# Performance work log

Measured on AMD Instinct MI355X. Metric: run time of the kernel, lower is better.

Reference implementation:

```python
import jax, jax.numpy as jnp
import numpy as np

R = 0.4          # ball radius
K = 32           # max_neighbors
S = 512          # cluster_num
BN_EPS = 1e-5


def fps(data, npoint):
    """Furthest point sampling. data: [B,N,C] -> idx [B,npoint] int32.
    Deterministic start at index 0 (original uses randint)."""
    B, N, C = data.shape

    def step(carry, _):
        dist, far = carry
        cent = jnp.take_along_axis(data, far[:, None, None], axis=1)  # [B,1,C]
        d = jnp.sum((data - cent) ** 2, -1)                           # [B,N]
        dist = jnp.minimum(dist, d)
        new_far = jnp.argmax(dist, -1).astype(jnp.int32)
        return (dist, new_far), far

    dist0 = jnp.full((B, N), 1e10, data.dtype)
    far0 = jnp.zeros((B,), jnp.int32)
    _, idxs = jax.lax.scan(step, (dist0, far0), None, length=npoint)
    return idxs.T  # [B,npoint]


def gather_points(data, idx):
    """data [B,N,C], idx [B,S] -> [B,S,C]"""
    return jnp.take_along_axis(data, idx[..., None], axis=1)


def gather_groups(data, idx):
    """data [B,N,C], idx [B,S,K] -> [B,S,K,C]"""
    B, N, C = data.shape
    _, Sq, Kq = idx.shape
    flat = jnp.take_along_axis(data, idx.reshape(B, Sq * Kq)[..., None], axis=1)
    return flat.reshape(B, Sq, Kq, C)


def square_dist(a, b):
    """a [B,N,C], b [B,M,C] -> [B,N,M]"""
    return (-2.0 * jnp.einsum('bnc,bmc->bnm', a, b)
            + jnp.sum(a ** 2, -1)[:, :, None]
            + jnp.sum(b ** 2, -1)[:, None, :])


def knn_query(data, query, max_neighbors, r):
    """Ball query: indices of up to max_neighbors points within r, padded with
    the first valid index. data [B,N,C], query [B,S,C] -> [B,S,K] int32."""
    B, N, _ = data.shape
    d = square_dist(query, data)                              # [B,S,N]
    idx = jnp.where(d <= r * r, jnp.arange(N, dtype=jnp.int32)[None, None, :], N)
    idx = jnp.sort(idx, axis=-1)[:, :, :max_neighbors]        # ascending, N = invalid
    first = idx[:, :, :1]
    return jnp.where(idx == N, first, idx)


def mlp_layer(x, w, b, g, be):
    """1x1 Conv2d + BatchNorm2d (training-mode batch stats) + ReLU.
    x [B,S,K,Cin], w [Cout,Cin] -> [B,S,K,Cout]"""
    y = jnp.einsum('bskc,oc->bsko', x, w) + b
    m = jnp.mean(y, axis=(0, 1, 2))
    v = jnp.var(y, axis=(0, 1, 2))
    y = (y - m) * jax.lax.rsqrt(v + BN_EPS) * g + be
    return jax.nn.relu(y)


def setup_inputs() -> dict:
    key = jax.random.key(0)
    ks = jax.random.split(key, 5)
    B, N = 16, 8192
    data = jax.random.normal(ks[0], (B, N, 3), jnp.float32)
    data_feature = jax.random.normal(ks[1], (B, N, 3), jnp.float32)
    w0 = jax.random.normal(ks[2], (64, 6), jnp.float32) * 0.1
    w1 = jax.random.normal(ks[3], (64, 64), jnp.float32) * 0.1
    w2 = jax.random.normal(ks[4], (128, 64), jnp.float32) * 0.1
    zeros = lambda c: jnp.zeros((c,), jnp.float32)
    ones = lambda c: jnp.ones((c,), jnp.float32)
    return dict(data=data, data_feature=data_feature,
                w0=w0, b0=zeros(64), g0=ones(64), be0=zeros(64),
                w1=w1, b1=zeros(64), g1=ones(64), be1=zeros(64),
                w2=w2, b2=zeros(128), g2=ones(128), be2=zeros(128))


def reference(data, data_feature, w0, b0, g0, be0, w1, b1, g1, be1, w2, b2, g2, be2):
    B, N, C = data.shape
    fps_idx = fps(data, S)                              # [B,S]
    centroids = gather_points(data, fps_idx)            # [B,S,3]
    nbr_idx = knn_query(data, centroids, K, R)          # [B,S,K]
    sample = gather_groups(data, nbr_idx)               # [B,S,K,3]
    sample_norm = sample - centroids[:, :, None, :]
    feat = gather_groups(data_feature, nbr_idx)         # [B,S,K,3]
    x = jnp.concatenate([sample_norm, feat], axis=-1)   # [B,S,K,6]
    x = mlp_layer(x, w0, b0, g0, be0)
    x = mlp_layer(x, w1, b1, g1, be1)
    x = mlp_layer(x, w2, b2, g2, be2)
    out = jnp.max(x, axis=2)                            # [B,S,128]
    return centroids, out
```

## Files before the change

### kernel.cpp

```cpp
#include <hip/hip_runtime.h>
#include <math.h>

constexpr int Bc = 16;
constexpr int Nc = 8192;
constexpr int Sc = 512;
constexpr int Kc = 32;
constexpr int Pc = Bc * Sc * Kc;

__global__ __launch_bounds__(256, 1)
void fps_kernel(const float* __restrict__ data,
                float* __restrict__ cent_out,
                float* __restrict__ cent_ws) {
  const int b = blockIdx.x;
  const int t = threadIdx.x;
  const int lane = t & 63, w = t >> 6;

  __shared__ float lx[Nc], ly[Nc], lz[Nc];
  __shared__ unsigned long long red_k[2][4];
  __shared__ int idx_hist[Sc];

  const float* db = data + (size_t)b * Nc * 3;

  float px[32], py[32], pz[32], dist[32];
#pragma unroll
  for (int j = 0; j < 32; ++j) {
    int p = t + 256 * j;
    px[j] = db[p * 3 + 0];
    py[j] = db[p * 3 + 1];
    pz[j] = db[p * 3 + 2];
    dist[j] = 1e10f;
    lx[p] = px[j]; ly[p] = py[j]; lz[p] = pz[j];
  }
  __syncthreads();

  int far = 0;
  for (int it = 0; it < Sc; ++it) {
    const int sfar = __builtin_amdgcn_readfirstlane(far);
    if (t == 0) idx_hist[it] = sfar;
    const float cx = lx[sfar];
    const float cy = ly[sfar];
    const float cz = lz[sfar];

    float best = -1.0f; int bj = 0;
#pragma unroll
    for (int j = 0; j < 32; ++j) {
      float dx = __fsub_rn(px[j], cx);
      float dy = __fsub_rn(py[j], cy);
      float dz = __fsub_rn(pz[j], cz);
      float d = __fadd_rn(__fadd_rn(__fmul_rn(dx, dx), __fmul_rn(dy, dy)),
                          __fmul_rn(dz, dz));
      float nd = fminf(dist[j], d);
      dist[j] = nd;
      if (nd > best) { best = nd; bj = j; }
    }
    const int bidx = t + 256 * bj;

    float wmax = best;
#pragma unroll
    for (int off = 32; off; off >>= 1) wmax = fmaxf(wmax, __shfl_xor(wmax, off));

    unsigned long long m = __ballot(best == wmax);
    int idx;
    if (__popcll(m) == 1) {
      idx = __shfl(bidx, (int)__ffsll((long long)m) - 1);
    } else {
      int cand = (best == wmax) ? bidx : 0x7fffffff;
#pragma unroll
      for (int off = 32; off; off >>= 1) cand = min(cand, __shfl_xor(cand, off));
      idx = cand;
    }

    unsigned long long key =
        ((unsigned long long)__float_as_uint(wmax) << 32) |
        (unsigned long long)(0xFFFFFFFFu - (unsigned)idx);
    const int par = it & 1;
    if (lane == 0) red_k[par][w] = key;
    __syncthreads();

    unsigned long long kk = red_k[par][lane & 3];
    {
      unsigned long long o1 = __shfl_xor(kk, 1);
      kk = (o1 > kk) ? o1 : kk;
      unsigned long long o2 = __shfl_xor(kk, 2);
      kk = (o2 > kk) ? o2 : kk;
    }
    far = (int)(0xFFFFFFFFu - (unsigned)(kk & 0xFFFFFFFFull));
  }

  __syncthreads();
  for (int s = t; s < Sc; s += 256) {
    int id = idx_hist[s];
    float cx = lx[id], cy = ly[id], cz = lz[id];
    size_t o = ((size_t)b * Sc + s) * 3;
    cent_out[o + 0] = cx; cent_out[o + 1] = cy; cent_out[o + 2] = cz;
    cent_ws[o + 0]  = cx; cent_ws[o + 1]  = cy; cent_ws[o + 2]  = cz;
  }
}

__global__ __launch_bounds__(256)
void ball_kernel(const float* __restrict__ data,
                 const float* __restrict__ feat,
                 const float* __restrict__ cent_ws,
                 float* __restrict__ x0) {
  const int w = threadIdx.x >> 6, lane = threadIdx.x & 63;
  const int q = blockIdx.x * 4 + w;
  const int b = q >> 9;
  const float* db = data + (size_t)b * Nc * 3;
  const float* fb = feat + (size_t)b * Nc * 3;

  const float qx = cent_ws[q * 3 + 0];
  const float qy = cent_ws[q * 3 + 1];
  const float qz = cent_ws[q * 3 + 2];
  const float q2 = __fadd_rn(__fadd_rn(__fmul_rn(qx, qx), __fmul_rn(qy, qy)),
                             __fmul_rn(qz, qz));

  __shared__ int nbr[4][Kc];
  int have = 0;
  for (int base = 0; base < Nc; base += 64) {
    int i = base + lane;
    float px = db[i * 3 + 0], py = db[i * 3 + 1], pz = db[i * 3 + 2];
    float p2 = __fadd_rn(__fadd_rn(__fmul_rn(px, px), __fmul_rn(py, py)),
                         __fmul_rn(pz, pz));
    float dt = fmaf(qz, pz, fmaf(qy, py, __fmul_rn(qx, px)));
    float d = __fadd_rn(__fadd_rn(__fmul_rn(-2.0f, dt), q2), p2);
    bool ok = d <= 0.16f;
    unsigned long long mask = __ballot(ok);
    if (mask) {
      int pos = have + __popcll(mask & ((1ull << lane) - 1ull));
      if (ok && pos < Kc) nbr[w][pos] = i;
      have += __popcll(mask);
      if (have >= Kc) break;
    }
  }
  if (have > Kc) have = Kc;
  __syncthreads();

  if (lane < Kc) {
    int k = lane;
    int j = nbr[w][k < have ? k : 0];
    float sx = __fsub_rn(db[j * 3 + 0], qx);
    float sy = __fsub_rn(db[j * 3 + 1], qy);
    float sz = __fsub_rn(db[j * 3 + 2], qz);
    float fx = fb[j * 3 + 0], fy = fb[j * 3 + 1], fz = fb[j * 3 + 2];
    size_t pidx = (size_t)q * Kc + k;
    x0[(size_t)0 * Pc + pidx] = sx;
    x0[(size_t)1 * Pc + pidx] = sy;
    x0[(size_t)2 * Pc + pidx] = sz;
    x0[(size_t)3 * Pc + pidx] = fx;
    x0[(size_t)4 * Pc + pidx] = fy;
    x0[(size_t)5 * Pc + pidx] = fz;
  }
}

__global__ __launch_bounds__(256)
void pass_a(const float* __restrict__ x0, const float* __restrict__ w0,
            const float* __restrict__ b0, float* __restrict__ part0) {
  const int lane = threadIdx.x & 63, w = threadIdx.x >> 6;
  const int slice = blockIdx.x * 4 + w;
  const int o = lane;
  float W[6];
#pragma unroll
  for (int c = 0; c < 6; ++c) W[c] = w0[o * 6 + c];
  const float bias = b0[o];
  float sum = 0.f, sq = 0.f;
  const int pps = Pc / 4096;
  const int p0 = slice * pps;
  for (int j = 0; j < pps; ++j) {
    int p = p0 + j;
    float y = bias;
#pragma unroll
    for (int c = 0; c < 6; ++c) y = fmaf(x0[(size_t)c * Pc + p], W[c], y);
    sum += y;
    sq = fmaf(y, y, sq);
  }
  __shared__ float bsum[64], bsq[64];
  if (threadIdx.x < 64) { bsum[threadIdx.x] = 0.f; bsq[threadIdx.x] = 0.f; }
  __syncthreads();
  atomicAdd(&bsum[o], sum);
  atomicAdd(&bsq[o], sq);
  __syncthreads();
  if (threadIdx.x < 64)       part0[blockIdx.x * 128 + threadIdx.x] = bsum[threadIdx.x];
  else if (threadIdx.x < 128) part0[blockIdx.x * 128 + threadIdx.x] = bsq[threadIdx.x - 64];
}

__global__ __launch_bounds__(256)
void reduce_k(const float* __restrict__ part, int nblk, int nch,
              const float* __restrict__ g, const float* __restrict__ be,
              float* __restrict__ AB) {
  const int o = blockIdx.x;
  const int t = threadIdx.x;
  double sum = 0.0, sq = 0.0;
  for (int i = t; i < nblk; i += 256) {
    sum += (double)part[(size_t)i * (2 * nch) + o];
    sq  += (double)part[(size_t)i * (2 * nch) + nch + o];
  }
  __shared__ double ls[256], lq[256];
  ls[t] = sum; lq[t] = sq;
  __syncthreads();
  for (int s = 128; s > 0; s >>= 1) {
    if (t < s) { ls[t] += ls[t + s]; lq[t] += lq[t + s]; }
    __syncthreads();
  }
  if (t == 0) {
    double m = ls[0] / (double)Pc;
    double v = lq[0] / (double)Pc - m * m;
    double A = (double)g[o] / sqrt(v + 1e-5);
    AB[o] = (float)A;
    AB[nch + o] = (float)((double)be[o] - m * A);
  }
}

__global__ __launch_bounds__(256)
void pass_b(const float* __restrict__ x0, const float* __restrict__ w0,
            const float* __restrict__ b0, const float* __restrict__ AB0,
            const float* __restrict__ w1, const float* __restrict__ b1,
            float* __restrict__ y1, float* __restrict__ part1) {
  const int p = blockIdx.x * 256 + threadIdx.x;
  const int lane = threadIdx.x & 63, w = threadIdx.x >> 6;

  float xin[6];
#pragma unroll
  for (int c = 0; c < 6; ++c) xin[c] = x0[(size_t)c * Pc + p];

  float x1[64];
#pragma unroll
  for (int o = 0; o < 64; ++o) {
    float y = b0[o];
#pragma unroll
    for (int c = 0; c < 6; ++c) y = fmaf(xin[c], w0[o * 6 + c], y);
    x1[o] = fmaxf(fmaf(y, AB0[o], AB0[64 + o]), 0.f);
  }

  __shared__ float ssum[4][64][17], ssq[4][64][17];

  for (int o = 0; o < 64; ++o) {
    float a0 = b1[o], a1 = 0.f, a2 = 0.f, a3 = 0.f;
#pragma unroll
    for (int c = 0; c < 64; c += 4) {
      a0 = fmaf(x1[c + 0], w1[o * 64 + c + 0], a0);
      a1 = fmaf(x1[c + 1], w1[o * 64 + c + 1], a1);
      a2 = fmaf(x1[c + 2], w1[o * 64 + c + 2], a2);
      a3 = fmaf(x1[c + 3], w1[o * 64 + c + 3], a3);
    }
    float acc = (a0 + a1) + (a2 + a3);
    y1[(size_t)o * Pc + p] = acc;

    float sv = acc + __shfl_xor(acc, 1);
    sv += __shfl_xor(sv, 2);
    float q = acc * acc;
    float qv = q + __shfl_xor(q, 1);
    qv += __shfl_xor(qv, 2);
    if ((lane & 3) == 0) {
      ssum[w][o][lane >> 2] = sv;
      ssq[w][o][lane >> 2] = qv;
    }
  }
  __syncthreads();
  if (threadIdx.x < 128) {
    const int o = threadIdx.x & 63;
    const bool isq = threadIdx.x >= 64;
    float s = 0.f;
#pragma unroll
    for (int ww = 0; ww < 4; ++ww)
      for (int k = 0; k < 16; ++k)
        s += isq ? ssq[ww][o][k] : ssum[ww][o][k];
    part1[blockIdx.x * 128 + threadIdx.x] = s;
  }
}

__global__ __launch_bounds__(256)
void pass_c(const float* __restrict__ y1, const float* __restrict__ AB1,
            const float* __restrict__ w2, const float* __restrict__ b2,
            float* __restrict__ maxy2, float* __restrict__ part2) {
  const int p = blockIdx.x * 256 + threadIdx.x;
  const int lane = threadIdx.x & 63, w = threadIdx.x >> 6;
  const int grp = p >> 5;

  float x2[64];
#pragma unroll
  for (int c = 0; c < 64; ++c) {
    float v = y1[(size_t)c * Pc + p];
    x2[c] = fmaxf(fmaf(v, AB1[c], AB1[64 + c]), 0.f);
  }

  __shared__ float ssum[4][128][9], ssq[4][128][9];

  for (int o = 0; o < 128; ++o) {
    float a0 = b2[o], a1 = 0.f, a2 = 0.f, a3 = 0.f;
#pragma unroll
    for (int c = 0; c < 64; c += 4) {
      a0 = fmaf(x2[c + 0], w2[o * 64 + c + 0], a0);
      a1 = fmaf(x2[c + 1], w2[o * 64 + c + 1], a1);
      a2 = fmaf(x2[c + 2], w2[o * 64 + c + 2], a2);
      a3 = fmaf(x2[c + 3], w2[o * 64 + c + 3], a3);
    }
    float acc = (a0 + a1) + (a2 + a3);

    float mx = acc;
#pragma unroll
    for (int off = 16; off > 0; off >>= 1) mx = fmaxf(mx, __shfl_xor(mx, off));
    if ((lane & 31) == 0) maxy2[(size_t)grp * 128 + o] = mx;

    float sv = acc + __shfl_xor(acc, 1);
    sv += __shfl_xor(sv, 2);
    sv += __shfl_xor(sv, 4);
    float q = acc * acc;
    float qv = q + __shfl_xor(q, 1);
    qv += __shfl_xor(qv, 2);
    qv += __shfl_xor(qv, 4);
    if ((lane & 7) == 0) {
      ssum[w][o][lane >> 3] = sv;
      ssq[w][o][lane >> 3] = qv;
    }
  }
  __syncthreads();
  {
    const int o = threadIdx.x & 127;
    const bool isq = threadIdx.x >= 128;
    float s = 0.f;
#pragma unroll
    for (int ww = 0; ww < 4; ++ww)
      for (int k = 0; k < 8; ++k)
        s += isq ? ssq[ww][o][k] : ssum[ww][o][k];
    part2[blockIdx.x * 256 + threadIdx.x] = s;
  }
}

__global__ __launch_bounds__(256)
void final_k(const float* __restrict__ maxy2, const float* __restrict__ AB2,
             float* __restrict__ out) {
  int i = blockIdx.x * 256 + threadIdx.x;
  int o = i & 127;
  out[i] = fmaxf(fmaf(maxy2[i], AB2[o], AB2[128 + o]), 0.f);
}

extern "C" void kernel_launch(void* const* d_in, const int* in_sizes, int n_in,
                              void* d_out, int out_size, void* d_ws, size_t ws_size,
                              hipStream_t stream) {
  const float* data = (const float*)d_in[0];
  const float* feat = (const float*)d_in[1];
  const float* w0 = (const float*)d_in[2];
  const float* b0 = (const float*)d_in[3];
  const float* g0 = (const float*)d_in[4];
  const float* be0 = (const float*)d_in[5];
  const float* w1 = (const float*)d_in[6];
  const float* b1 = (const float*)d_in[7];
  const float* g1 = (const float*)d_in[8];
  const float* be1 = (const float*)d_in[9];
  const float* w2 = (const float*)d_in[10];
  const float* b2 = (const float*)d_in[11];
  const float* g2 = (const float*)d_in[12];
  const float* be2 = (const float*)d_in[13];
  float* out = (float*)d_out;

  float* ws = (float*)d_ws;
  float* cent_ws = ws; ws += (size_t)Bc * Sc * 3;
  float* x0 = ws;      ws += (size_t)6 * Pc;
  float* y1 = ws;      ws += (size_t)64 * Pc;
  float* maxy2 = ws;   ws += (size_t)Bc * Sc * 128;
  float* part0 = ws;   ws += 1024 * 128;
  float* part1 = ws;   ws += 1024 * 128;
  float* part2 = ws;   ws += 1024 * 256;
  float* AB0 = ws;     ws += 128;
  float* AB1 = ws;     ws += 128;
  float* AB2 = ws;     ws += 256;

  fps_kernel<<<Bc, 256, 0, stream>>>(data, out, cent_ws);
  ball_kernel<<<(Bc * Sc) / 4, 256, 0, stream>>>(data, feat, cent_ws, x0);
  pass_a<<<1024, 256, 0, stream>>>(x0, w0, b0, part0);
  reduce_k<<<64, 256, 0, stream>>>(part0, 1024, 64, g0, be0, AB0);
  pass_b<<<Pc / 256, 256, 0, stream>>>(x0, w0, b0, AB0, w1, b1, y1, part1);
  reduce_k<<<64, 256, 0, stream>>>(part1, 1024, 64, g1, be1, AB1);
  pass_c<<<Pc / 256, 256, 0, stream>>>(y1, AB1, w2, b2, maxy2, part2);
  reduce_k<<<128, 256, 0, stream>>>(part2, 1024, 128, g2, be2, AB2);
  final_k<<<(Bc * Sc * 128) / 256, 256, 0, stream>>>(maxy2, AB2, out + (size_t)Bc * Sc * 3);
}
```

Measured before the change: 869.3 us.

## Recompute layer-1 activations in pass_c instead of storing y1; DPP reductions in FPS

```diff
diff --git a/kernel.cpp b/kernel.cpp
--- a/kernel.cpp
+++ b/kernel.cpp
@@ -6,6 +6,12 @@
 constexpr int Sc = 512;
 constexpr int Kc = 32;
 constexpr int Pc = Bc * Sc * Kc;
+
+template <int CTRL>
+__device__ __forceinline__ float dpp_max_stage(float x) {
+  int p = __builtin_amdgcn_update_dpp(0, __float_as_int(x), CTRL, 0xf, 0xf, true);
+  return fmaxf(x, __int_as_float(p));
+}
 
 __global__ __launch_bounds__(256, 1)
 void fps_kernel(const float* __restrict__ data,
@@ -56,8 +62,12 @@
     const int bidx = t + 256 * bj;
 
     float wmax = best;
-#pragma unroll
-    for (int off = 32; off; off >>= 1) wmax = fmaxf(wmax, __shfl_xor(wmax, off));
+    wmax = dpp_max_stage<0xB1>(wmax);
+    wmax = dpp_max_stage<0x4E>(wmax);
+    wmax = dpp_max_stage<0x141>(wmax);
+    wmax = dpp_max_stage<0x140>(wmax);
+    wmax = fmaxf(wmax, __shfl_xor(wmax, 16));
+    wmax = fmaxf(wmax, __shfl_xor(wmax, 32));
 
     unsigned long long m = __ballot(best == wmax);
     int idx;
@@ -77,13 +87,13 @@
     if (lane == 0) red_k[par][w] = key;
     __syncthreads();
 
-    unsigned long long kk = red_k[par][lane & 3];
-    {
-      unsigned long long o1 = __shfl_xor(kk, 1);
-      kk = (o1 > kk) ? o1 : kk;
-      unsigned long long o2 = __shfl_xor(kk, 2);
-      kk = (o2 > kk) ? o2 : kk;
-    }
+    unsigned long long k0 = red_k[par][0];
+    unsigned long long k1 = red_k[par][1];
+    unsigned long long k2 = red_k[par][2];
+    unsigned long long k3 = red_k[par][3];
+    unsigned long long ka = (k0 > k1) ? k0 : k1;
+    unsigned long long kb = (k2 > k3) ? k2 : k3;
+    unsigned long long kk = (ka > kb) ? ka : kb;
     far = (int)(0xFFFFFFFFu - (unsigned)(kk & 0xFFFFFFFFull));
   }
 
@@ -214,7 +224,7 @@
 void pass_b(const float* __restrict__ x0, const float* __restrict__ w0,
             const float* __restrict__ b0, const float* __restrict__ AB0,
             const float* __restrict__ w1, const float* __restrict__ b1,
-            float* __restrict__ y1, float* __restrict__ part1) {
+            float* __restrict__ part1) {
   const int p = blockIdx.x * 256 + threadIdx.x;
   const int lane = threadIdx.x & 63, w = threadIdx.x >> 6;
 
@@ -243,7 +253,6 @@
       a3 = fmaf(x1[c + 3], w1[o * 64 + c + 3], a3);
     }
     float acc = (a0 + a1) + (a2 + a3);
-    y1[(size_t)o * Pc + p] = acc;
 
     float sv = acc + __shfl_xor(acc, 1);
     sv += __shfl_xor(sv, 2);
@@ -269,18 +278,42 @@
 }
 
 __global__ __launch_bounds__(256)
-void pass_c(const float* __restrict__ y1, const float* __restrict__ AB1,
+void pass_c(const float* __restrict__ x0, const float* __restrict__ w0,
+            const float* __restrict__ b0, const float* __restrict__ AB0,
+            const float* __restrict__ w1, const float* __restrict__ b1,
+            const float* __restrict__ AB1,
             const float* __restrict__ w2, const float* __restrict__ b2,
             float* __restrict__ maxy2, float* __restrict__ part2) {
   const int p = blockIdx.x * 256 + threadIdx.x;
   const int lane = threadIdx.x & 63, w = threadIdx.x >> 6;
   const int grp = p >> 5;
 
+  float xin[6];
+#pragma unroll
+  for (int c = 0; c < 6; ++c) xin[c] = x0[(size_t)c * Pc + p];
+
+  float x1[64];
+#pragma unroll
+  for (int o = 0; o < 64; ++o) {
+    float y = b0[o];
+#pragma unroll
+    for (int c = 0; c < 6; ++c) y = fmaf(xin[c], w0[o * 6 + c], y);
+    x1[o] = fmaxf(fmaf(y, AB0[o], AB0[64 + o]), 0.f);
+  }
+
   float x2[64];
 #pragma unroll
-  for (int c = 0; c < 64; ++c) {
-    float v = y1[(size_t)c * Pc + p];
-    x2[c] = fmaxf(fmaf(v, AB1[c], AB1[64 + c]), 0.f);
+  for (int o = 0; o < 64; ++o) {
+    float a0 = b1[o], a1 = 0.f, a2 = 0.f, a3 = 0.f;
+#pragma unroll
+    for (int c = 0; c < 64; c += 4) {
+      a0 = fmaf(x1[c + 0], w1[o * 64 + c + 0], a0);
+      a1 = fmaf(x1[c + 1], w1[o * 64 + c + 1], a1);
+      a2 = fmaf(x1[c + 2], w1[o * 64 + c + 2], a2);
+      a3 = fmaf(x1[c + 3], w1[o * 64 + c + 3], a3);
+    }
+    float acc = (a0 + a1) + (a2 + a3);
+    x2[o] = fmaxf(fmaf(acc, AB1[o], AB1[64 + o]), 0.f);
   }
 
   __shared__ float ssum[4][128][9], ssq[4][128][9];
@@ -356,7 +389,6 @@
   float* ws = (float*)d_ws;
   float* cent_ws = ws; ws += (size_t)Bc * Sc * 3;
   float* x0 = ws;      ws += (size_t)6 * Pc;
-  float* y1 = ws;      ws += (size_t)64 * Pc;
   float* maxy2 = ws;   ws += (size_t)Bc * Sc * 128;
   float* part0 = ws;   ws += 1024 * 128;
   float* part1 = ws;   ws += 1024 * 128;
@@ -369,9 +401,10 @@
   ball_kernel<<<(Bc * Sc) / 4, 256, 0, stream>>>(data, feat, cent_ws, x0);
   pass_a<<<1024, 256, 0, stream>>>(x0, w0, b0, part0);
   reduce_k<<<64, 256, 0, stream>>>(part0, 1024, 64, g0, be0, AB0);
-  pass_b<<<Pc / 256, 256, 0, stream>>>(x0, w0, b0, AB0, w1, b1, y1, part1);
+  pass_b<<<Pc / 256, 256, 0, stream>>>(x0, w0, b0, AB0, w1, b1, part1);
   reduce_k<<<64, 256, 0, stream>>>(part1, 1024, 64, g1, be1, AB1);
-  pass_c<<<Pc / 256, 256, 0, stream>>>(y1, AB1, w2, b2, maxy2, part2);
+  pass_c<<<Pc / 256, 256, 0, stream>>>(x0, w0, b0, AB0, w1, b1, AB1, w2, b2,
+                                       maxy2, part2);
   reduce_k<<<128, 256, 0, stream>>>(part2, 1024, 128, g2, be2, AB2);
   final_k<<<(Bc * Sc * 128) / 256, 256, 0, stream>>>(maxy2, AB2, out + (size_t)Bc * Sc * 3);
 }
```

After: 940.7 us. 1.08x slower.
